# Kernel tuning notes

Hardware: AMD Instinct MI355X
Metric: run time of the kernel (lower is better)

The kernel has to match this reference:

```python
import jax, jax.numpy as jnp
import numpy as np

IN_CHANNELS = 8
OUT_CHANNELS = 32
KERNEL_SIZE = 5
BATCH = 16
H = W = 128


def setup_inputs() -> dict:
    key = jax.random.key(0)
    k_in, k_hit, k_miss = jax.random.split(key, 3)
    x = jax.random.normal(k_in, (BATCH, IN_CHANNELS, H, W), dtype=jnp.float32)
    stdv = 1.0 / np.sqrt(IN_CHANNELS * KERNEL_SIZE ** 2)
    K_hit = jax.random.uniform(k_hit, (OUT_CHANNELS, IN_CHANNELS, KERNEL_SIZE, KERNEL_SIZE),
                               minval=-stdv, maxval=stdv, dtype=jnp.float32)
    K_miss = jax.random.uniform(k_miss, (OUT_CHANNELS, IN_CHANNELS, KERNEL_SIZE, KERNEL_SIZE),
                                minval=-stdv, maxval=stdv, dtype=jnp.float32)
    return {"input": x, "K_hit": K_hit, "K_miss": K_miss}


def _hitmiss(x, K_hit, K_miss):
    # x: [B,C,H,W]; K_*: [O,C,k,k]
    # out[b,o,y,x] = min_{c,u,v}(x[b,c,y+u,x+v] - K_hit[o,c,u,v])
    #             - max_{c,u,v}(x[b,c,y+u,x+v] - K_miss[o,c,u,v])
    # (torch code computes F_hit = maxpool(-(patch - K_hit)) so -F_hit = min(patch - K_hit),
    #  F_miss = maxpool(patch - K_miss); output = -F_hit - F_miss.)
    B, C, Hh, Ww = x.shape
    O, _, k, _ = K_hit.shape
    fh = Hh - k + 1
    hit_min = jnp.full((B, O, fh, fh), jnp.inf, dtype=x.dtype)
    miss_max = jnp.full((B, O, fh, fh), -jnp.inf, dtype=x.dtype)
    for u in range(k):  # fixed small loop over kernel offsets (k*k = 25)
        for v in range(k):
            win = x[:, :, u:u + fh, v:v + fh]          # [B,C,fh,fh]
            win_b = win[:, None]                        # [B,1,C,fh,fh]
            dh = win_b - K_hit[None, :, :, u, v, None, None]   # [B,O,C,fh,fh]
            dm = win_b - K_miss[None, :, :, u, v, None, None]
            hit_min = jnp.minimum(hit_min, dh.min(axis=2))
            miss_max = jnp.maximum(miss_max, dm.max(axis=2))
    return hit_min - miss_max


def reference(input, K_hit, K_miss):
    return _hitmiss(input, K_hit, K_miss)
```

## Files before the change

kernel.cpp:

```cpp
#include <hip/hip_runtime.h>
#include <math.h>

constexpr int IC   = 8;
constexpr int OC   = 32;
constexpr int KS   = 5;
constexpr int B_   = 16;
constexpr int HW_  = 128;
constexpr int FH   = 124;
constexpr int KTAP = KS * KS;
constexpr int OG   = 4;
constexpr int OPG  = 8;

typedef _Float16 h2 __attribute__((ext_vector_type(2)));

__global__ void pack_k_kernel(const float* __restrict__ Kh,
                              const float* __restrict__ Km,
                              unsigned* __restrict__ Kpk) {
    int idx = blockIdx.x * 256 + threadIdx.x;
    if (idx >= IC * OG * KTAP * 2 * OPG) return;
    int oi = idx & 7;
    int h  = (idx >> 3) & 1;
    int t  = (idx >> 4) % KTAP;
    int cg = (idx >> 4) / KTAP;
    int g  = cg & (OG - 1), c = cg >> 2;
    int o  = g * OPG + oi;
    const float* K = h ? Km : Kh;
    float k = -K[(o * IC + c) * KTAP + t];
    _Float16 nk = (_Float16)k;
    unsigned short us = __builtin_bit_cast(unsigned short, nk);
    Kpk[idx] = (unsigned)us | ((unsigned)us << 16);
}

__global__ __launch_bounds__(64, 6) void hitmiss_f16_kernel(
    const float* __restrict__ x,
    const unsigned* __restrict__ Kpk,
    float* __restrict__ out)
{
    const int lane = threadIdx.x;
    const int i = blockIdx.x, b = blockIdx.y, g = blockIdx.z;
    const int j0 = lane * 2;
    if (j0 >= FH) return;

    h2 hit[OPG], miss[OPG];
    const h2 pinf = {(_Float16)INFINITY, (_Float16)INFINITY};
    const h2 ninf = {(_Float16)(-INFINITY), (_Float16)(-INFINITY)};
#pragma unroll
    for (int oi = 0; oi < OPG; ++oi) { hit[oi] = pinf; miss[oi] = ninf; }

#pragma unroll 1
    for (int c = 0; c < IC; ++c) {
        const float* xp = x + (((b * IC + c) * HW_) + i) * HW_ + j0;
        h2 xpk[KTAP];
#pragma unroll
        for (int u = 0; u < KS; ++u) {
            const float2 f0 = *(const float2*)(xp + u * HW_);
            const float2 f1 = *(const float2*)(xp + u * HW_ + 2);
            const float2 f2 = *(const float2*)(xp + u * HW_ + 4);
            const float fv[6] = {f0.x, f0.y, f1.x, f1.y, f2.x, f2.y};
#pragma unroll
            for (int v = 0; v < KS; ++v)
                xpk[u * KS + v] = __builtin_bit_cast(h2,
                    __builtin_amdgcn_cvt_pkrtz(fv[v], fv[v + 1]));
        }
        const unsigned* kc = Kpk + (size_t)((c * OG + g) * KTAP) * 2 * OPG;
#pragma unroll
        for (int t = 0; t < KTAP; ++t) {
#pragma unroll
            for (int oi = 0; oi < OPG; ++oi) {
                const h2 nh = __builtin_bit_cast(h2, kc[t * 16 + oi]);
                const h2 nm = __builtin_bit_cast(h2, kc[t * 16 + 8 + oi]);
                hit[oi]  = __builtin_elementwise_min(xpk[t] + nh, hit[oi]);
                miss[oi] = __builtin_elementwise_max(xpk[t] + nm, miss[oi]);
            }
        }
    }

#pragma unroll
    for (int oi = 0; oi < OPG; ++oi) {
        const h2 r = hit[oi] - miss[oi];
        const int o = g * OPG + oi;
        float* op = out + (((size_t)b * OC + o) * FH + i) * FH + j0;
        op[0] = (float)r[0];
        op[1] = (float)r[1];
    }
}

__global__ __launch_bounds__(128) void hitmiss_f32_kernel(
    const float* __restrict__ x,
    const float* __restrict__ Kh,
    const float* __restrict__ Km,
    float* __restrict__ out)
{
    const int j = threadIdx.x;
    const int i = blockIdx.x;
    const int b = blockIdx.y;
    if (j >= FH) return;

    float hit[OC], miss[OC];
#pragma unroll
    for (int o = 0; o < OC; ++o) { hit[o] = INFINITY; miss[o] = -INFINITY; }

#pragma unroll 1
    for (int c = 0; c < IC; ++c) {
        const float* xp = x + (((b * IC + c) * HW_) + i) * HW_ + j;
        float xw[KTAP];
#pragma unroll
        for (int u = 0; u < KS; ++u)
#pragma unroll
            for (int v = 0; v < KS; ++v)
                xw[u * KS + v] = xp[u * HW_ + v];
#pragma unroll
        for (int t = 0; t < KTAP - 1; t += 2) {
            const float x0 = xw[t], x1 = xw[t + 1];
#pragma unroll
            for (int o = 0; o < OC; ++o) {
                const float kh0 = Kh[(o * IC + c) * KTAP + t];
                const float kh1 = Kh[(o * IC + c) * KTAP + t + 1];
                const float km0 = Km[(o * IC + c) * KTAP + t];
                const float km1 = Km[(o * IC + c) * KTAP + t + 1];
                hit[o]  = fminf(fminf(x0 - kh0, x1 - kh1), hit[o]);
                miss[o] = fmaxf(fmaxf(x0 - km0, x1 - km1), miss[o]);
            }
        }
        {
            const float x0 = xw[KTAP - 1];
#pragma unroll
            for (int o = 0; o < OC; ++o) {
                hit[o]  = fminf(hit[o],  x0 - Kh[(o * IC + c) * KTAP + KTAP - 1]);
                miss[o] = fmaxf(miss[o], x0 - Km[(o * IC + c) * KTAP + KTAP - 1]);
            }
        }
    }

    float* op = out + ((size_t)(b * OC) * FH + i) * FH + j;
#pragma unroll
    for (int o = 0; o < OC; ++o)
        op[(size_t)o * FH * FH] = hit[o] - miss[o];
}

extern "C" void kernel_launch(void* const* d_in, const int* in_sizes, int n_in,
                              void* d_out, int out_size, void* d_ws, size_t ws_size,
                              hipStream_t stream) {
    const float* x  = (const float*)d_in[0];
    const float* Kh = (const float*)d_in[1];
    const float* Km = (const float*)d_in[2];
    float* out = (float*)d_out;

    const size_t kdwords = (size_t)IC * OG * KTAP * 2 * OPG;
    if (ws_size >= kdwords * sizeof(unsigned)) {
        unsigned* Kpk = (unsigned*)d_ws;
        pack_k_kernel<<<(int)((kdwords + 255) / 256), 256, 0, stream>>>(Kh, Km, Kpk);
        dim3 grid(FH, B_, OG);
        hitmiss_f16_kernel<<<grid, 64, 0, stream>>>(x, Kpk, out);
    } else {
        dim3 grid(FH, B_);
        hitmiss_f32_kernel<<<grid, 128, 0, stream>>>(x, Kh, Km, out);
    }
}
```

Measured before the change: 168.7 us.

## Stage packed fp16 input rows in double-buffered LDS shared across four output rows

Each block now computes four output rows with four wavefronts. The input rows for each channel are converted to packed half2 pairs (even and odd offsets) once and stored in LDS. The next channel is prefetched into registers and written to the other buffer, so the global loads and conversions no longer repeat for every output row. In exchange, the kernel adds __syncthreads per channel and LDS traffic, and it rolls the u loop, which may cost some instruction-level parallelism.

```diff
diff --git a/kernel.cpp b/kernel.cpp
--- a/kernel.cpp
+++ b/kernel.cpp
@@ -10,8 +10,16 @@
 constexpr int KTAP = KS * KS;
 constexpr int OG   = 4;
 constexpr int OPG  = 8;
+constexpr int RPB  = 4;
+constexpr int XR   = RPB + KS - 1;
+constexpr int DW   = HW_ / 2;
 
 typedef _Float16 h2 __attribute__((ext_vector_type(2)));
+
+__device__ __forceinline__ h2 bc2(unsigned u) { return __builtin_bit_cast(h2, u); }
+__device__ __forceinline__ unsigned pkf(float a, float b) {
+    return __builtin_bit_cast(unsigned, __builtin_amdgcn_cvt_pkrtz(a, b));
+}
 
 __global__ void pack_k_kernel(const float* __restrict__ Kh,
                               const float* __restrict__ Km,
@@ -31,15 +39,22 @@
     Kpk[idx] = (unsigned)us | ((unsigned)us << 16);
 }
 
-__global__ __launch_bounds__(64, 6) void hitmiss_f16_kernel(
+__global__ __launch_bounds__(256, 6) void hitmiss_lds_kernel(
     const float* __restrict__ x,
     const unsigned* __restrict__ Kpk,
     float* __restrict__ out)
 {
-    const int lane = threadIdx.x;
-    const int i = blockIdx.x, b = blockIdx.y, g = blockIdx.z;
+    __shared__ unsigned lds[2 * 2 * XR * DW + 16];
+    const int tid  = threadIdx.x;
+    const int lane = tid & 63;
+    const int w    = tid >> 6;
+    const int ibase = blockIdx.x * RPB;
+    const int b = blockIdx.y, g = blockIdx.z;
     const int j0 = lane * 2;
-    if (j0 >= FH) return;
+
+    const int sr = tid >> 5;
+    const int sq = tid & 31;
+    const int scol = sq * 4;
 
     h2 hit[OPG], miss[OPG];
     const h2 pinf = {(_Float16)INFINITY, (_Float16)INFINITY};
@@ -47,41 +62,71 @@
 #pragma unroll
     for (int oi = 0; oi < OPG; ++oi) { hit[oi] = pinf; miss[oi] = ninf; }
 
+    {
+        const float* xr = x + (((size_t)(b * IC + 0) * HW_) + ibase + sr) * HW_ + scol;
+        const float4 f = *(const float4*)xr;
+        const float f4 = (scol + 4 < HW_) ? xr[4] : 0.f;
+        const int ba = 0 * 2 * XR * DW + sr * DW + 2 * sq;
+        lds[ba]     = pkf(f.x, f.y);
+        lds[ba + 1] = pkf(f.z, f.w);
+        lds[ba + XR * DW]     = pkf(f.y, f.z);
+        lds[ba + XR * DW + 1] = pkf(f.w, f4);
+    }
+
 #pragma unroll 1
     for (int c = 0; c < IC; ++c) {
-        const float* xp = x + (((b * IC + c) * HW_) + i) * HW_ + j0;
-        h2 xpk[KTAP];
-#pragma unroll
+        __syncthreads();
+        const int buf = c & 1;
+
+        float4 nf = {0.f, 0.f, 0.f, 0.f};
+        float nf4 = 0.f;
+        if (c + 1 < IC) {
+            const float* xr = x + (((size_t)(b * IC + (c + 1)) * HW_) + ibase + sr) * HW_ + scol;
+            nf = *(const float4*)xr;
+            if (scol + 4 < HW_) nf4 = xr[4];
+        }
+
+        const unsigned* kc = Kpk + (size_t)((c * OG + g) * KTAP) * 16;
+#pragma unroll 1
         for (int u = 0; u < KS; ++u) {
-            const float2 f0 = *(const float2*)(xp + u * HW_);
-            const float2 f1 = *(const float2*)(xp + u * HW_ + 2);
-            const float2 f2 = *(const float2*)(xp + u * HW_ + 4);
-            const float fv[6] = {f0.x, f0.y, f1.x, f1.y, f2.x, f2.y};
-#pragma unroll
-            for (int v = 0; v < KS; ++v)
-                xpk[u * KS + v] = __builtin_bit_cast(h2,
-                    __builtin_amdgcn_cvt_pkrtz(fv[v], fv[v + 1]));
-        }
-        const unsigned* kc = Kpk + (size_t)((c * OG + g) * KTAP) * 2 * OPG;
-#pragma unroll
-        for (int t = 0; t < KTAP; ++t) {
-#pragma unroll
-            for (int oi = 0; oi < OPG; ++oi) {
-                const h2 nh = __builtin_bit_cast(h2, kc[t * 16 + oi]);
-                const h2 nm = __builtin_bit_cast(h2, kc[t * 16 + 8 + oi]);
-                hit[oi]  = __builtin_elementwise_min(xpk[t] + nh, hit[oi]);
-                miss[oi] = __builtin_elementwise_max(xpk[t] + nm, miss[oi]);
+            const unsigned* ku = kc + u * KS * 16;
+            const int ra = buf * 2 * XR * DW + (w + u) * DW + lane;
+            const h2 xv[KS] = {
+                bc2(lds[ra]),
+                bc2(lds[ra + XR * DW]),
+                bc2(lds[ra + 1]),
+                bc2(lds[ra + XR * DW + 1]),
+                bc2(lds[ra + 2]) };
+#pragma unroll
+            for (int v = 0; v < KS; ++v) {
+#pragma unroll
+                for (int oi = 0; oi < OPG; ++oi) {
+                    const h2 nh = bc2(ku[v * 16 + oi]);
+                    const h2 nm = bc2(ku[v * 16 + 8 + oi]);
+                    hit[oi]  = __builtin_elementwise_min(xv[v] + nh, hit[oi]);
+                    miss[oi] = __builtin_elementwise_max(xv[v] + nm, miss[oi]);
+                }
             }
         }
-    }
-
-#pragma unroll
-    for (int oi = 0; oi < OPG; ++oi) {
-        const h2 r = hit[oi] - miss[oi];
-        const int o = g * OPG + oi;
-        float* op = out + (((size_t)b * OC + o) * FH + i) * FH + j0;
-        op[0] = (float)r[0];
-        op[1] = (float)r[1];
+
+        if (c + 1 < IC) {
+            const int ba = (buf ^ 1) * 2 * XR * DW + sr * DW + 2 * sq;
+            lds[ba]     = pkf(nf.x, nf.y);
+            lds[ba + 1] = pkf(nf.z, nf.w);
+            lds[ba + XR * DW]     = pkf(nf.y, nf.z);
+            lds[ba + XR * DW + 1] = pkf(nf.w, nf4);
+        }
+    }
+
+    if (j0 < FH) {
+        const int i0 = ibase + w;
+#pragma unroll
+        for (int oi = 0; oi < OPG; ++oi) {
+            const h2 res = hit[oi] - miss[oi];
+            const int o = g * OPG + oi;
+            float2 st; st.x = (float)res[0]; st.y = (float)res[1];
+            *(float2*)(out + (((size_t)b * OC + o) * FH + i0) * FH + j0) = st;
+        }
     }
 }
 
@@ -150,8 +195,8 @@
     if (ws_size >= kdwords * sizeof(unsigned)) {
         unsigned* Kpk = (unsigned*)d_ws;
         pack_k_kernel<<<(int)((kdwords + 255) / 256), 256, 0, stream>>>(Kh, Km, Kpk);
-        dim3 grid(FH, B_, OG);
-        hitmiss_f16_kernel<<<grid, 64, 0, stream>>>(x, Kpk, out);
+        dim3 grid(FH / RPB, B_, OG);
+        hitmiss_lds_kernel<<<grid, 256, 0, stream>>>(x, Kpk, out);
     } else {
         dim3 grid(FH, B_);
         hitmiss_f32_kernel<<<grid, 128, 0, stream>>>(x, Kh, Km, out);
```

After: 178.0 us. +5.5%, slower.

## Pre-pack input into fp16 pair layouts and use two-row blocks

Applied to the files above, without the earlier changes.

Adds a pre-pass that converts x into two packed-half2 buffers (even-aligned and odd-shifted pairs), so the main kernel loads ready-made h2 operands instead of converting floats per channel row. The main kernel now runs two output rows per 128-thread block and writes results with float2 stores. This trades an extra pass over the input and a larger workspace for fewer conversions and loads in the hot loop. It only runs when the workspace is large enough, otherwise the older paths are used.

```diff
diff --git a/kernel.cpp b/kernel.cpp
--- a/kernel.cpp
+++ b/kernel.cpp
@@ -10,8 +10,15 @@
 constexpr int KTAP = KS * KS;
 constexpr int OG   = 4;
 constexpr int OPG  = 8;
+constexpr int DW   = HW_ / 2;
+constexpr size_t NXD = (size_t)B_ * IC * HW_ * DW;
 
 typedef _Float16 h2 __attribute__((ext_vector_type(2)));
+
+__device__ __forceinline__ h2 bc2(unsigned u) { return __builtin_bit_cast(h2, u); }
+__device__ __forceinline__ unsigned pkf(float a, float b) {
+    return __builtin_bit_cast(unsigned, __builtin_amdgcn_cvt_pkrtz(a, b));
+}
 
 __global__ void pack_k_kernel(const float* __restrict__ Kh,
                               const float* __restrict__ Km,
@@ -31,6 +38,74 @@
     Kpk[idx] = (unsigned)us | ((unsigned)us << 16);
 }
 
+__global__ void pack_x_kernel(const float* __restrict__ x,
+                              unsigned* __restrict__ wsA) {
+    unsigned* wsB = wsA + NXD;
+    size_t idx = (size_t)blockIdx.x * 256 + threadIdx.x;
+    if (idx >= NXD) return;
+    int m = (int)(idx & (DW - 1));
+    size_t row = idx >> 6;
+    const float* xr = x + row * HW_ + 2 * m;
+    float a0 = xr[0], a1 = xr[1];
+    float a2 = (m < DW - 1) ? xr[2] : 0.f;
+    wsA[idx] = pkf(a0, a1);
+    wsB[idx] = pkf(a1, a2);
+}
+
+__global__ __launch_bounds__(128, 8) void hitmiss_pk_kernel(
+    const unsigned* __restrict__ xpk,
+    const unsigned* __restrict__ Kpk,
+    float* __restrict__ out)
+{
+    const int lane = threadIdx.x & 63;
+    const int w    = threadIdx.x >> 6;
+    const int i = blockIdx.x * 2 + w;
+    const int b = blockIdx.y, g = blockIdx.z;
+    const int j0 = lane * 2;
+
+    h2 hit[OPG], miss[OPG];
+    const h2 pinf = {(_Float16)INFINITY, (_Float16)INFINITY};
+    const h2 ninf = {(_Float16)(-INFINITY), (_Float16)(-INFINITY)};
+#pragma unroll
+    for (int oi = 0; oi < OPG; ++oi) { hit[oi] = pinf; miss[oi] = ninf; }
+
+    const unsigned* rbase = xpk + ((size_t)(b * IC) * HW_ + i) * DW + lane;
+
+#pragma unroll 1
+    for (int c = 0; c < IC; ++c) {
+        const unsigned* kc = Kpk + (size_t)((c * OG + g) * KTAP) * 16;
+        const unsigned* rc = rbase + (size_t)c * HW_ * DW;
+#pragma unroll
+        for (int u = 0; u < KS; ++u) {
+            const unsigned* ra = rc + u * DW;
+            const h2 xv[KS] = { bc2(ra[0]),       bc2(ra[NXD]),
+                                bc2(ra[1]),       bc2(ra[NXD + 1]),
+                                bc2(ra[2]) };
+            const unsigned* ku = kc + u * KS * 16;
+#pragma unroll
+            for (int v = 0; v < KS; ++v) {
+#pragma unroll
+                for (int oi = 0; oi < OPG; ++oi) {
+                    const h2 nh = bc2(ku[v * 16 + oi]);
+                    const h2 nm = bc2(ku[v * 16 + 8 + oi]);
+                    hit[oi]  = __builtin_elementwise_min(xv[v] + nh, hit[oi]);
+                    miss[oi] = __builtin_elementwise_max(xv[v] + nm, miss[oi]);
+                }
+            }
+        }
+    }
+
+    if (j0 < FH) {
+#pragma unroll
+        for (int oi = 0; oi < OPG; ++oi) {
+            const h2 res = hit[oi] - miss[oi];
+            const int o = g * OPG + oi;
+            float2 st; st.x = (float)res[0]; st.y = (float)res[1];
+            *(float2*)(out + (((size_t)b * OC + o) * FH + i) * FH + j0) = st;
+        }
+    }
+}
+
 __global__ __launch_bounds__(64, 6) void hitmiss_f16_kernel(
     const float* __restrict__ x,
     const unsigned* __restrict__ Kpk,
@@ -62,13 +137,13 @@
                 xpk[u * KS + v] = __builtin_bit_cast(h2,
                     __builtin_amdgcn_cvt_pkrtz(fv[v], fv[v + 1]));
         }
-        const unsigned* kc = Kpk + (size_t)((c * OG + g) * KTAP) * 2 * OPG;
+        const unsigned* kc = Kpk + (size_t)((c * OG + g) * KTAP) * 16;
 #pragma unroll
         for (int t = 0; t < KTAP; ++t) {
 #pragma unroll
             for (int oi = 0; oi < OPG; ++oi) {
-                const h2 nh = __builtin_bit_cast(h2, kc[t * 16 + oi]);
-                const h2 nm = __builtin_bit_cast(h2, kc[t * 16 + 8 + oi]);
+                const h2 nh = bc2(kc[t * 16 + oi]);
+                const h2 nm = bc2(kc[t * 16 + 8 + oi]);
                 hit[oi]  = __builtin_elementwise_min(xpk[t] + nh, hit[oi]);
                 miss[oi] = __builtin_elementwise_max(xpk[t] + nm, miss[oi]);
             }
@@ -77,11 +152,11 @@
 
 #pragma unroll
     for (int oi = 0; oi < OPG; ++oi) {
-        const h2 r = hit[oi] - miss[oi];
+        const h2 res = hit[oi] - miss[oi];
         const int o = g * OPG + oi;
         float* op = out + (((size_t)b * OC + o) * FH + i) * FH + j0;
-        op[0] = (float)r[0];
-        op[1] = (float)r[1];
+        op[0] = (float)res[0];
+        op[1] = (float)res[1];
     }
 }
 
@@ -110,24 +185,12 @@
             for (int v = 0; v < KS; ++v)
                 xw[u * KS + v] = xp[u * HW_ + v];
 #pragma unroll
-        for (int t = 0; t < KTAP - 1; t += 2) {
-            const float x0 = xw[t], x1 = xw[t + 1];
+        for (int t = 0; t < KTAP; ++t) {
+            const float x0 = xw[t];
 #pragma unroll
             for (int o = 0; o < OC; ++o) {
-                const float kh0 = Kh[(o * IC + c) * KTAP + t];
-                const float kh1 = Kh[(o * IC + c) * KTAP + t + 1];
-                const float km0 = Km[(o * IC + c) * KTAP + t];
-                const float km1 = Km[(o * IC + c) * KTAP + t + 1];
-                hit[o]  = fminf(fminf(x0 - kh0, x1 - kh1), hit[o]);
-                miss[o] = fmaxf(fmaxf(x0 - km0, x1 - km1), miss[o]);
-            }
-        }
-        {
-            const float x0 = xw[KTAP - 1];
-#pragma unroll
-            for (int o = 0; o < OC; ++o) {
-                hit[o]  = fminf(hit[o],  x0 - Kh[(o * IC + c) * KTAP + KTAP - 1]);
-                miss[o] = fmaxf(miss[o], x0 - Km[(o * IC + c) * KTAP + KTAP - 1]);
+                hit[o]  = fminf(hit[o],  x0 - Kh[(o * IC + c) * KTAP + t]);
+                miss[o] = fmaxf(miss[o], x0 - Km[(o * IC + c) * KTAP + t]);
             }
         }
     }
@@ -147,7 +210,16 @@
     float* out = (float*)d_out;
 
     const size_t kdwords = (size_t)IC * OG * KTAP * 2 * OPG;
-    if (ws_size >= kdwords * sizeof(unsigned)) {
+    const size_t need_full = (2 * NXD + kdwords) * sizeof(unsigned);
+
+    if (ws_size >= need_full) {
+        unsigned* wsA = (unsigned*)d_ws;
+        unsigned* Kpk = wsA + 2 * NXD;
+        pack_k_kernel<<<(int)((kdwords + 255) / 256), 256, 0, stream>>>(Kh, Km, Kpk);
+        pack_x_kernel<<<(int)(NXD / 256), 256, 0, stream>>>(x, wsA);
+        dim3 grid(FH / 2, B_, OG);
+        hitmiss_pk_kernel<<<grid, 128, 0, stream>>>(wsA, Kpk, out);
+    } else if (ws_size >= kdwords * sizeof(unsigned)) {
         unsigned* Kpk = (unsigned*)d_ws;
         pack_k_kernel<<<(int)((kdwords + 255) / 256), 256, 0, stream>>>(Kh, Km, Kpk);
         dim3 grid(FH, B_, OG);
```

New measurement: 177.3 us. 1.05x slower.
